# Optimization experiments

Hardware: AMD Instinct MI355X
Metric: run time of the kernel (lower is better)

Reference implementation:

```python
import jax, jax.numpy as jnp
import numpy as np

P, F_IN, HG, C, T, E, HOUT = 4096, 64, 64, 64, 32, 65536, 12
LEAKY_SLOPE = 0.2
LN_EPS = 1e-5


def setup_inputs() -> dict:
    key = jax.random.key(0)
    ks = jax.random.split(key, 14)
    g = lambda k, shape, scale: (jax.random.normal(k, shape, jnp.float32) * scale)
    return {
        "X": jax.random.normal(ks[0], (1, P, F_IN, T), jnp.float32),
        "edge_index": jax.random.randint(ks[1], (T, 2, E), 0, P, jnp.int32),
        # GATv2 params (single head)
        "Wl": g(ks[2], (F_IN, HG), 0.1),
        "Wr": g(ks[3], (F_IN, HG), 0.1),
        "att": g(ks[4], (HG,), 0.1),
        "gat_b": g(ks[5], (HG,), 0.02),
        # 1x1 time conv (HG -> C) and 1x1 residual conv (F_IN -> C)
        "W_time": g(ks[6], (C, HG), 0.1),
        "b_time": g(ks[7], (C,), 0.02),
        "W_res": g(ks[8], (C, F_IN), 0.1),
        "b_res": g(ks[9], (C,), 0.02),
        # LayerNorm over channel dim C
        "ln_g": jnp.ones((C,), jnp.float32),
        "ln_b": jnp.zeros((C,), jnp.float32),
        # final conv: Conv2d(in=T, out=HOUT, kernel=(1, C)) -> weight (HOUT, T, C)
        "W_final": g(ks[10], (HOUT, T, C), 0.05),
        "b_final": g(ks[11], (HOUT,), 0.02),
    }


def reference(X, edge_index, Wl, Wr, att, gat_b, W_time, b_time, W_res, b_res,
              ln_g, ln_b, W_final, b_final):
    Pn = X.shape[1]

    def gat_t(x, edges):
        # x: (P, F_IN), edges: (2, E) with edges[0]=src j, edges[1]=dst i
        src, dst = edges[0], edges[1]
        hl = x @ Wl                      # (P, HG) messages
        hr = x @ Wr                      # (P, HG) query side
        e = jax.nn.leaky_relu(hl[src] + hr[dst], LEAKY_SLOPE) @ att  # (E,)
        emax = jax.ops.segment_max(e, dst, num_segments=Pn)
        ex = jnp.exp(e - emax[dst])
        den = jax.ops.segment_sum(ex, dst, num_segments=Pn)
        alpha = ex / den[dst]            # softmax over in-edges of each dst
        return jax.ops.segment_sum(alpha[:, None] * hl[src], dst,
                                   num_segments=Pn) + gat_b  # (P, HG)

    xs = jnp.moveaxis(X[0], -1, 0)                     # (T, P, F_IN)
    X_hat = jax.nn.relu(jax.vmap(gat_t)(xs, edge_index))  # (T, P, HG)

    th = jnp.einsum('tph,ch->tpc', X_hat, W_time) + b_time  # time conv 1x1
    rs = jnp.einsum('tpf,cf->tpc', xs, W_res) + b_res       # residual conv 1x1
    y = jax.nn.relu(th + rs)                                 # (T, P, C)

    mu = jnp.mean(y, axis=-1, keepdims=True)
    var = jnp.var(y, axis=-1, keepdims=True)
    yn = (y - mu) * jax.lax.rsqrt(var + LN_EPS) * ln_g + ln_b  # (T, P, C)

    # final conv: in-channels = T, kernel (1, C) -> contract over t and c
    out = jnp.einsum('tpc,otc->po', yn, W_final) + b_final     # (P, HOUT)
    return out[None]                                           # (1, P, HOUT)
```

## Files before the change

### kernel.cpp

```cpp
#include <hip/hip_runtime.h>
#include <math.h>

#define NP 4096
#define F_IN 64
#define HG 64
#define NC 64
#define NT 32
#define NE 65536
#define HOUT 12
#define LEAKY 0.2f
#define LN_EPS 1e-5f
#define CAPC 32

template <int CTRL>
__device__ __forceinline__ float dppadd(float v, float x) {
    int r = __builtin_amdgcn_update_dpp(0, __builtin_bit_cast(int, x), CTRL, 0xF, 0xF, false);
    return v + __builtin_bit_cast(float, r);
}
__device__ __forceinline__ float rowsum16(float v) {
    v = dppadd<0x128>(v, v);
    v = dppadd<0x124>(v, v);
    v = dppadd<0x122>(v, v);
    v = dppadd<0x121>(v, v);
    return v;
}
__device__ __forceinline__ float laneXorSum(float v) {
    v += __shfl_xor(v, 16, 64);
    v += __shfl_xor(v, 32, 64);
    return v;
}

#define FMA4(Acomp, B, r)                                                     \
    acc[r][0] += (Acomp) * (B).x; acc[r][1] += (Acomp) * (B).y;               \
    acc[r][2] += (Acomp) * (B).z; acc[r][3] += (Acomp) * (B).w;

__global__ __launch_bounds__(256) void k_front(const float* __restrict__ X,
        const float* __restrict__ Wl, const float* __restrict__ Wr,
        const float* __restrict__ W_res, const float* __restrict__ b_res,
        const float* __restrict__ W_time,
        const int* __restrict__ EI,
        float* __restrict__ hl, float* __restrict__ hr, float* __restrict__ rs,
        float* __restrict__ wtT,
        int* __restrict__ cnt, unsigned short* __restrict__ scap) {
    __shared__ float smem[8960];
    int b = blockIdx.x;
    int tid = threadIdx.x;
    if (b < 512) {
        unsigned short (*buck)[CAPC] = (unsigned short (*)[CAPC])smem;
        int* cnts = (int*)(smem + 8192);
        int t = (b & 7) + 8 * ((b >> 3) & 3);
        int rem = b >> 5;
        int c = rem & 1, r = rem >> 1;
        cnts[tid] = 0; cnts[tid + 256] = 0;
        __syncthreads();
        const int4* srcA = (const int4*)(EI + (size_t)t * 2 * NE) + c * (NE / 8);
        const int4* dstA = (const int4*)(EI + (size_t)t * 2 * NE + NE) + c * (NE / 8);
        for (int i = tid; i < NE / 8; i += 256) {
            int4 s = srcA[i];
            int4 d = dstA[i];
            if ((d.x >> 9) == r) { int lo = d.x & 511; int sl = atomicAdd(&cnts[lo], 1); if (sl < CAPC) buck[lo][sl] = (unsigned short)s.x; }
            if ((d.y >> 9) == r) { int lo = d.y & 511; int sl = atomicAdd(&cnts[lo], 1); if (sl < CAPC) buck[lo][sl] = (unsigned short)s.y; }
            if ((d.z >> 9) == r) { int lo = d.z & 511; int sl = atomicAdd(&cnts[lo], 1); if (sl < CAPC) buck[lo][sl] = (unsigned short)s.z; }
            if ((d.w >> 9) == r) { int lo = d.w & 511; int sl = atomicAdd(&cnts[lo], 1); if (sl < CAPC) buck[lo][sl] = (unsigned short)s.w; }
        }
        __syncthreads();
        int obase = ((t * 2 + c) << 12) + (r << 9);
        cnt[obase + tid] = cnts[tid];
        cnt[obase + tid + 256] = cnts[tid + 256];
        unsigned int* dstw = (unsigned int*)(scap + (size_t)obase * CAPC);
        const unsigned int* srcw = (const unsigned int*)buck;
        for (int i = tid; i < 512 * CAPC / 2; i += 256)
            dstw[i] = srcw[i];
    } else if (b < 2560) {
        float (*xs)[F_IN][36] = (float (*)[F_IN][36])smem;
        float (*bk)[68] = (float (*)[68])(smem + 4608);
        int p0 = (b - 512) * 2;
        const float4* Xp = (const float4*)(X + (size_t)p0 * F_IN * NT);
        for (int i4 = tid; i4 < 1024; i4 += 256) {
            int pp = i4 >> 9, f = (i4 >> 3) & 63, t0 = (i4 & 7) * 4;
            *(float4*)&xs[pp][f][t0] = Xp[i4];
        }
        int ng = tid & 15, pp = (tid >> 4) & 1, tg = tid >> 5;
        int n0 = ng * 4, t0 = tg * 4;
        {
            const float4* B4 = (const float4*)Wl;
            for (int i4 = tid; i4 < 1024; i4 += 256)
                *(float4*)&bk[i4 >> 4][(i4 & 15) * 4] = B4[i4];
            __syncthreads();
            float acc[4][4];
#pragma unroll
            for (int i = 0; i < 4; ++i)
#pragma unroll
                for (int j2 = 0; j2 < 4; ++j2) acc[i][j2] = 0.f;
#pragma unroll 8
            for (int f = 0; f < F_IN; ++f) {
                float4 B = *(const float4*)&bk[f][n0];
                float4 A = *(const float4*)&xs[pp][f][t0];
                FMA4(A.x, B, 0) FMA4(A.y, B, 1) FMA4(A.z, B, 2) FMA4(A.w, B, 3)
            }
#pragma unroll
            for (int i = 0; i < 4; ++i) {
                float4 v;
                v.x = acc[i][0]; v.y = acc[i][1]; v.z = acc[i][2]; v.w = acc[i][3];
                *(float4*)&hl[((size_t)(t0 + i) * NP + p0 + pp) * HG + n0] = v;
            }
            __syncthreads();
        }
        {
            const float4* B4 = (const float4*)Wr;
            for (int i4 = tid; i4 < 1024; i4 += 256)
                *(float4*)&bk[i4 >> 4][(i4 & 15) * 4] = B4[i4];
            __syncthreads();
            float acc[4][4];
#pragma unroll
            for (int i = 0; i < 4; ++i)
#pragma unroll
                for (int j2 = 0; j2 < 4; ++j2) acc[i][j2] = 0.f;
#pragma unroll 8
            for (int f = 0; f < F_IN; ++f) {
                float4 B = *(const float4*)&bk[f][n0];
                float4 A = *(const float4*)&xs[pp][f][t0];
                FMA4(A.x, B, 0) FMA4(A.y, B, 1) FMA4(A.z, B, 2) FMA4(A.w, B, 3)
            }
#pragma unroll
            for (int i = 0; i < 4; ++i) {
                float4 v;
                v.x = acc[i][0]; v.y = acc[i][1]; v.z = acc[i][2]; v.w = acc[i][3];
                *(float4*)&hr[((size_t)(t0 + i) * NP + p0 + pp) * HG + n0] = v;
            }
            __syncthreads();
        }
        {
            for (int i = tid; i < F_IN * NC; i += 256) {
                int c = i >> 6, f = i & 63;
                bk[f][c] = W_res[i];
            }
            __syncthreads();
            float4 br4 = *(const float4*)&b_res[n0];
            float acc[4][4];
#pragma unroll
            for (int i = 0; i < 4; ++i) {
                acc[i][0] = br4.x; acc[i][1] = br4.y; acc[i][2] = br4.z; acc[i][3] = br4.w;
            }
#pragma unroll 8
            for (int f = 0; f < F_IN; ++f) {
                float4 B = *(const float4*)&bk[f][n0];
                float4 A = *(const float4*)&xs[pp][f][t0];
                FMA4(A.x, B, 0) FMA4(A.y, B, 1) FMA4(A.z, B, 2) FMA4(A.w, B, 3)
            }
#pragma unroll
            for (int i = 0; i < 4; ++i) {
                float4 v;
                v.x = acc[i][0]; v.y = acc[i][1]; v.z = acc[i][2]; v.w = acc[i][3];
                *(float4*)&rs[((size_t)(t0 + i) * NP + p0 + pp) * NC + n0] = v;
            }
        }
    } else {
        int i = (b - 2560) * 256 + tid;
        wtT[i] = W_time[(i & 63) * 64 + (i >> 6)];
    }
}

__global__ __launch_bounds__(256) void k_gat(const float* __restrict__ hl,
        const float* __restrict__ hr, const float* __restrict__ rs,
        const int* __restrict__ cnt, const unsigned short* __restrict__ scap,
        const float* __restrict__ att, const float* __restrict__ gat_b,
        const float* __restrict__ wtT, const float* __restrict__ b_time,
        const float* __restrict__ ln_g, const float* __restrict__ ln_b,
        const float* __restrict__ Wf, float* __restrict__ pout) {
    __shared__ int sidx[4][64];
    __shared__ float xbuf[4][64];
    int b = blockIdx.x;
    int t = (b & 7) + 8 * (b >> 10);
    int pc = (b >> 3) & 127;
    int ws = threadIdx.x >> 6;
    int lane = threadIdx.x & 63;
    int row = lane >> 4;
    int cg = lane & 15;
    int c0 = cg * 4;
    const float* hlt = hl + (size_t)t * NP * HG;
    float4 at4 = *(const float4*)&att[c0];
    float4 gb4 = *(const float4*)&gat_b[c0];
    float4 bt4 = *(const float4*)&b_time[c0];
    float4 lg  = *(const float4*)&ln_g[c0];
    float4 lb  = *(const float4*)&ln_b[c0];
    float4 wreg[16];
    {
        const float4* wq = (const float4*)wtT + (size_t)(row * 16) * (HG / 4) + cg;
#pragma unroll
        for (int i = 0; i < 16; ++i) wreg[i] = wq[i * (HG / 4)];
    }
    float4 wf0 = *(const float4*)&Wf[((size_t)(3 * row + 0) * NT + t) * NC + c0];
    float4 wf1 = *(const float4*)&Wf[((size_t)(3 * row + 1) * NT + t) * NC + c0];
    float4 wf2 = *(const float4*)&Wf[((size_t)(3 * row + 2) * NT + t) * NC + c0];

    for (int q = 0; q < 8; ++q) {
        int p = pc * 32 + ws * 8 + q;
        size_t nbase = ((size_t)t * NP + p) * HG;
        float4 r4 = *(const float4*)&hr[nbase + c0];
        int d0 = cnt[((t * 2 + 0) << 12) + p]; d0 = (d0 < CAPC) ? d0 : CAPC;
        int d1 = cnt[((t * 2 + 1) << 12) + p]; d1 = (d1 < CAPC) ? d1 : CAPC;
        int deg = d0 + d1;
        const unsigned short* s0 = scap + ((size_t)(((t * 2 + 0) << 12) + p)) * CAPC;
        const unsigned short* s1 = scap + ((size_t)(((t * 2 + 1) << 12) + p)) * CAPC;
        int li = (lane < deg) ? lane : 0;
        int f1 = (li >= d0);
        int idx = f1 ? (li - d0) : li;
        sidx[ws][lane] = (int)(f1 ? s1 : s0)[idx];
        float l = 0.f;
        float4 acc = {0.f, 0.f, 0.f, 0.f};
        int nfull = deg & ~7;
        int j = 0;
        for (; j < nfull; j += 8) {
            int src0 = sidx[ws][j + row];
            int src1 = sidx[ws][j + 4 + row];
            float4 h0 = *(const float4*)&hlt[((size_t)src0 << 6) + c0];
            float4 h1 = *(const float4*)&hlt[((size_t)src1 << 6) + c0];
            float4 z0, z1;
            z0.x = h0.x + r4.x; z0.y = h0.y + r4.y; z0.z = h0.z + r4.z; z0.w = h0.w + r4.w;
            z1.x = h1.x + r4.x; z1.y = h1.y + r4.y; z1.z = h1.z + r4.z; z1.w = h1.w + r4.w;
            z0.x = fmaxf(z0.x, LEAKY * z0.x); z0.y = fmaxf(z0.y, LEAKY * z0.y);
            z0.z = fmaxf(z0.z, LEAKY * z0.z); z0.w = fmaxf(z0.w, LEAKY * z0.w);
            z1.x = fmaxf(z1.x, LEAKY * z1.x); z1.y = fmaxf(z1.y, LEAKY * z1.y);
            z1.z = fmaxf(z1.z, LEAKY * z1.z); z1.w = fmaxf(z1.w, LEAKY * z1.w);
            float e0 = rowsum16(z0.x * at4.x + z0.y * at4.y + z0.z * at4.z + z0.w * at4.w);
            float e1 = rowsum16(z1.x * at4.x + z1.y * at4.y + z1.z * at4.z + z1.w * at4.w);
            float w0 = __expf(e0);
            float w1 = __expf(e1);
            l += w0 + w1;
            acc.x += w0 * h0.x + w1 * h1.x;
            acc.y += w0 * h0.y + w1 * h1.y;
            acc.z += w0 * h0.z + w1 * h1.z;
            acc.w += w0 * h0.w + w1 * h1.w;
        }
        for (; j < deg; j += 4) {
            int jj = j + row;
            int src = sidx[ws][(jj < deg) ? jj : 0];
            float4 ha = *(const float4*)&hlt[((size_t)src << 6) + c0];
            float4 za;
            za.x = ha.x + r4.x; za.y = ha.y + r4.y; za.z = ha.z + r4.z; za.w = ha.w + r4.w;
            za.x = fmaxf(za.x, LEAKY * za.x);
            za.y = fmaxf(za.y, LEAKY * za.y);
            za.z = fmaxf(za.z, LEAKY * za.z);
            za.w = fmaxf(za.w, LEAKY * za.w);
            float ep = za.x * at4.x + za.y * at4.y + za.z * at4.z + za.w * at4.w;
            float e = rowsum16(ep);
            float w = __expf(e);
            w = (jj < deg) ? w : 0.f;
            l += w;
            acc.x += w * ha.x; acc.y += w * ha.y; acc.z += w * ha.z; acc.w += w * ha.w;
        }
        float lt = laneXorSum(l);
        acc.x = laneXorSum(acc.x);
        acc.y = laneXorSum(acc.y);
        acc.z = laneXorSum(acc.z);
        acc.w = laneXorSum(acc.w);
        float inv = (deg > 0) ? (1.0f / lt) : 0.f;
        float4 xh;
        xh.x = fmaxf(acc.x * inv + gb4.x, 0.f);
        xh.y = fmaxf(acc.y * inv + gb4.y, 0.f);
        xh.z = fmaxf(acc.z * inv + gb4.z, 0.f);
        xh.w = fmaxf(acc.w * inv + gb4.w, 0.f);
        if (row == 0) *(float4*)&xbuf[ws][c0] = xh;
        float4 y4 = {0.f, 0.f, 0.f, 0.f};
#pragma unroll
        for (int i = 0; i < 16; ++i) {
            float xf = xbuf[ws][row * 16 + i];
            y4.x += xf * wreg[i].x; y4.y += xf * wreg[i].y;
            y4.z += xf * wreg[i].z; y4.w += xf * wreg[i].w;
        }
        y4.x = laneXorSum(y4.x); y4.y = laneXorSum(y4.y);
        y4.z = laneXorSum(y4.z); y4.w = laneXorSum(y4.w);
        float4 rs4 = *(const float4*)&rs[((size_t)t * NP + p) * NC + c0];
        float y0 = fmaxf(y4.x + bt4.x + rs4.x, 0.f);
        float y1 = fmaxf(y4.y + bt4.y + rs4.y, 0.f);
        float y2 = fmaxf(y4.z + bt4.z + rs4.z, 0.f);
        float y3 = fmaxf(y4.w + bt4.w + rs4.w, 0.f);
        float s  = rowsum16(y0 + y1 + y2 + y3);
        float ss = rowsum16(y0 * y0 + y1 * y1 + y2 * y2 + y3 * y3);
        float mu = s * (1.f / 64.f);
        float var = ss * (1.f / 64.f) - mu * mu;
        float rsd = rsqrtf(var + LN_EPS);
        float n0 = (y0 - mu) * rsd * lg.x + lb.x;
        float n1 = (y1 - mu) * rsd * lg.y + lb.y;
        float n2 = (y2 - mu) * rsd * lg.z + lb.z;
        float n3 = (y3 - mu) * rsd * lg.w + lb.w;
        float o0 = n0 * wf0.x + n1 * wf0.y + n2 * wf0.z + n3 * wf0.w;
        float o1 = n0 * wf1.x + n1 * wf1.y + n2 * wf1.z + n3 * wf1.w;
        float o2 = n0 * wf2.x + n1 * wf2.y + n2 * wf2.z + n3 * wf2.w;
        o0 = rowsum16(o0); o1 = rowsum16(o1); o2 = rowsum16(o2);
        if (cg == 0) {
            float* pp = pout + ((size_t)t * NP + p) * HOUT + 3 * row;
            pp[0] = o0; pp[1] = o1; pp[2] = o2;
        }
    }
}

__global__ __launch_bounds__(256) void k_out(const float* __restrict__ pout,
        const float* __restrict__ bf, float* __restrict__ out) {
    int k = blockIdx.x * 256 + threadIdx.x;
    float s = bf[k % HOUT];
#pragma unroll 8
    for (int t = 0; t < NT; ++t) s += pout[(size_t)t * (NP * HOUT) + k];
    out[k] = s;
}

extern "C" void kernel_launch(void* const* d_in, const int* in_sizes, int n_in,
                              void* d_out, int out_size, void* d_ws, size_t ws_size,
                              hipStream_t stream) {
    const float* X      = (const float*)d_in[0];
    const int*   EI     = (const int*)d_in[1];
    const float* Wl     = (const float*)d_in[2];
    const float* Wr     = (const float*)d_in[3];
    const float* att    = (const float*)d_in[4];
    const float* gat_b  = (const float*)d_in[5];
    const float* W_time = (const float*)d_in[6];
    const float* b_time = (const float*)d_in[7];
    const float* W_res  = (const float*)d_in[8];
    const float* b_res  = (const float*)d_in[9];
    const float* ln_g   = (const float*)d_in[10];
    const float* ln_b   = (const float*)d_in[11];
    const float* Wf     = (const float*)d_in[12];
    const float* bf     = (const float*)d_in[13];
    float* out = (float*)d_out;

    char* ws = (char*)d_ws;
    const size_t MB = 1024 * 1024;
    float* hl   = (float*)(ws);
    float* hr   = (float*)(ws + 32 * MB);
    float* rs   = (float*)(ws + 64 * MB);
    float* wtT  = (float*)(ws + 96 * MB);
    int*   cnt  = (int*)  (ws + 97 * MB);
    unsigned short* scap = (unsigned short*)(ws + 98 * MB);
    float* pout = (float*)(ws + 114 * MB);

    k_front<<<2576, 256, 0, stream>>>(X, Wl, Wr, W_res, b_res, W_time, EI,
                                      hl, hr, rs, wtT, cnt, scap);
    k_gat  <<<4096, 256, 0, stream>>>(hl, hr, rs, cnt, scap, att, gat_b,
                                      wtT, b_time, ln_g, ln_b, Wf, pout);
    k_out  <<<NP * HOUT / 256, 256, 0, stream>>>(pout, bf, out);
}
```

Before: 285.0 us.

## Restructure GAT kernel into phased per-warp batches with LDS weights and coalesced output

k_gat now prefetches the degrees and source indices for all 8 nodes of a wavefront into LDS up front. It then runs the attention aggregation for all 8 nodes, and afterwards does the time-conv matmul as one batched pass that reads the transposed W_time from LDS instead of holding 16 float4 registers per thread. Final per-node outputs are staged in LDS and written to pout as one contiguous store per wavefront instead of scattered 3-float writes. k_front's X tile padding changes from 36 to 40 floats. The intent is lower register pressure, better latency hiding and fewer small global stores, at the cost of more LDS use per block.

```diff
diff --git a/kernel.cpp b/kernel.cpp
--- a/kernel.cpp
+++ b/kernel.cpp
@@ -42,7 +42,7 @@
         float* __restrict__ hl, float* __restrict__ hr, float* __restrict__ rs,
         float* __restrict__ wtT,
         int* __restrict__ cnt, unsigned short* __restrict__ scap) {
-    __shared__ float smem[8960];
+    __shared__ float smem[9472];
     int b = blockIdx.x;
     int tid = threadIdx.x;
     if (b < 512) {
@@ -72,8 +72,8 @@
         for (int i = tid; i < 512 * CAPC / 2; i += 256)
             dstw[i] = srcw[i];
     } else if (b < 2560) {
-        float (*xs)[F_IN][36] = (float (*)[F_IN][36])smem;
-        float (*bk)[68] = (float (*)[68])(smem + 4608);
+        float (*xs)[F_IN][40] = (float (*)[F_IN][40])smem;
+        float (*bk)[68] = (float (*)[68])(smem + 5120);
         int p0 = (b - 512) * 2;
         const float4* Xp = (const float4*)(X + (size_t)p0 * F_IN * NT);
         for (int i4 = tid; i4 < 1024; i4 += 256) {
@@ -168,52 +168,60 @@
         const float* __restrict__ wtT, const float* __restrict__ b_time,
         const float* __restrict__ ln_g, const float* __restrict__ ln_b,
         const float* __restrict__ Wf, float* __restrict__ pout) {
-    __shared__ int sidx[4][64];
-    __shared__ float xbuf[4][64];
+    __shared__ int sidx[4][8][64];
+    __shared__ float xbuf[4][8][64];
+    __shared__ int sdeg[4][8];
+    __shared__ float wt[64][68];
     int b = blockIdx.x;
     int t = (b & 7) + 8 * (b >> 10);
     int pc = (b >> 3) & 127;
-    int ws = threadIdx.x >> 6;
-    int lane = threadIdx.x & 63;
+    int tid = threadIdx.x;
+    int ws = tid >> 6;
+    int lane = tid & 63;
     int row = lane >> 4;
     int cg = lane & 15;
     int c0 = cg * 4;
-    const float* hlt = hl + (size_t)t * NP * HG;
+    const float4* w4s = (const float4*)wtT;
+    for (int i4 = tid; i4 < 1024; i4 += 256)
+        *(float4*)&wt[i4 >> 4][(i4 & 15) * 4] = w4s[i4];
+    __syncthreads();
     float4 at4 = *(const float4*)&att[c0];
     float4 gb4 = *(const float4*)&gat_b[c0];
     float4 bt4 = *(const float4*)&b_time[c0];
     float4 lg  = *(const float4*)&ln_g[c0];
     float4 lb  = *(const float4*)&ln_b[c0];
-    float4 wreg[16];
-    {
-        const float4* wq = (const float4*)wtT + (size_t)(row * 16) * (HG / 4) + cg;
-#pragma unroll
-        for (int i = 0; i < 16; ++i) wreg[i] = wq[i * (HG / 4)];
-    }
     float4 wf0 = *(const float4*)&Wf[((size_t)(3 * row + 0) * NT + t) * NC + c0];
     float4 wf1 = *(const float4*)&Wf[((size_t)(3 * row + 1) * NT + t) * NC + c0];
     float4 wf2 = *(const float4*)&Wf[((size_t)(3 * row + 2) * NT + t) * NC + c0];
-
+    int p0 = pc * 32 + ws * 8;
+    const int* cb0 = cnt + ((t * 2 + 0) << 12) + p0;
+    const int* cb1 = cnt + ((t * 2 + 1) << 12) + p0;
+    const unsigned short* sb0 = scap + ((size_t)(((t * 2 + 0) << 12) + p0)) * CAPC;
+    const unsigned short* sb1 = scap + ((size_t)(((t * 2 + 1) << 12) + p0)) * CAPC;
+#pragma unroll
     for (int q = 0; q < 8; ++q) {
-        int p = pc * 32 + ws * 8 + q;
-        size_t nbase = ((size_t)t * NP + p) * HG;
-        float4 r4 = *(const float4*)&hr[nbase + c0];
-        int d0 = cnt[((t * 2 + 0) << 12) + p]; d0 = (d0 < CAPC) ? d0 : CAPC;
-        int d1 = cnt[((t * 2 + 1) << 12) + p]; d1 = (d1 < CAPC) ? d1 : CAPC;
+        int d0 = cb0[q]; d0 = (d0 < CAPC) ? d0 : CAPC;
+        int d1 = cb1[q]; d1 = (d1 < CAPC) ? d1 : CAPC;
         int deg = d0 + d1;
-        const unsigned short* s0 = scap + ((size_t)(((t * 2 + 0) << 12) + p)) * CAPC;
-        const unsigned short* s1 = scap + ((size_t)(((t * 2 + 1) << 12) + p)) * CAPC;
+        if (lane == 0) sdeg[ws][q] = deg;
         int li = (lane < deg) ? lane : 0;
         int f1 = (li >= d0);
         int idx = f1 ? (li - d0) : li;
-        sidx[ws][lane] = (int)(f1 ? s1 : s0)[idx];
+        const unsigned short* sp = f1 ? (sb1 + q * CAPC) : (sb0 + q * CAPC);
+        sidx[ws][q][lane] = (int)sp[idx];
+    }
+    const float* hlt = hl + (size_t)t * NP * HG;
+    for (int q = 0; q < 8; ++q) {
+        int p = p0 + q;
+        float4 r4 = *(const float4*)&hr[((size_t)t * NP + p) * HG + c0];
+        int deg = sdeg[ws][q];
         float l = 0.f;
         float4 acc = {0.f, 0.f, 0.f, 0.f};
         int nfull = deg & ~7;
         int j = 0;
         for (; j < nfull; j += 8) {
-            int src0 = sidx[ws][j + row];
-            int src1 = sidx[ws][j + 4 + row];
+            int src0 = sidx[ws][q][j + row];
+            int src1 = sidx[ws][q][j + 4 + row];
             float4 h0 = *(const float4*)&hlt[((size_t)src0 << 6) + c0];
             float4 h1 = *(const float4*)&hlt[((size_t)src1 << 6) + c0];
             float4 z0, z1;
@@ -235,7 +243,7 @@
         }
         for (; j < deg; j += 4) {
             int jj = j + row;
-            int src = sidx[ws][(jj < deg) ? jj : 0];
+            int src = sidx[ws][q][(jj < deg) ? jj : 0];
             float4 ha = *(const float4*)&hlt[((size_t)src << 6) + c0];
             float4 za;
             za.x = ha.x + r4.x; za.y = ha.y + r4.y; za.z = ha.z + r4.z; za.w = ha.w + r4.w;
@@ -261,21 +269,38 @@
         xh.y = fmaxf(acc.y * inv + gb4.y, 0.f);
         xh.z = fmaxf(acc.z * inv + gb4.z, 0.f);
         xh.w = fmaxf(acc.w * inv + gb4.w, 0.f);
-        if (row == 0) *(float4*)&xbuf[ws][c0] = xh;
-        float4 y4 = {0.f, 0.f, 0.f, 0.f};
-#pragma unroll
-        for (int i = 0; i < 16; ++i) {
-            float xf = xbuf[ws][row * 16 + i];
-            y4.x += xf * wreg[i].x; y4.y += xf * wreg[i].y;
-            y4.z += xf * wreg[i].z; y4.w += xf * wreg[i].w;
-        }
-        y4.x = laneXorSum(y4.x); y4.y = laneXorSum(y4.y);
-        y4.z = laneXorSum(y4.z); y4.w = laneXorSum(y4.w);
-        float4 rs4 = *(const float4*)&rs[((size_t)t * NP + p) * NC + c0];
-        float y0 = fmaxf(y4.x + bt4.x + rs4.x, 0.f);
-        float y1 = fmaxf(y4.y + bt4.y + rs4.y, 0.f);
-        float y2 = fmaxf(y4.z + bt4.z + rs4.z, 0.f);
-        float y3 = fmaxf(y4.w + bt4.w + rs4.w, 0.f);
+        if (row == 0) *(float4*)&xbuf[ws][q][c0] = xh;
+    }
+    float4 y[8];
+#pragma unroll
+    for (int q = 0; q < 8; ++q) { y[q].x = 0.f; y[q].y = 0.f; y[q].z = 0.f; y[q].w = 0.f; }
+#pragma unroll
+    for (int i4 = 0; i4 < 4; ++i4) {
+        int h0 = row * 16 + i4 * 4;
+        float4 w0 = *(const float4*)&wt[h0 + 0][c0];
+        float4 w1 = *(const float4*)&wt[h0 + 1][c0];
+        float4 w2 = *(const float4*)&wt[h0 + 2][c0];
+        float4 w3 = *(const float4*)&wt[h0 + 3][c0];
+#pragma unroll
+        for (int q = 0; q < 8; ++q) {
+            float4 xf = *(const float4*)&xbuf[ws][q][h0];
+            y[q].x += xf.x * w0.x + xf.y * w1.x + xf.z * w2.x + xf.w * w3.x;
+            y[q].y += xf.x * w0.y + xf.y * w1.y + xf.z * w2.y + xf.w * w3.y;
+            y[q].z += xf.x * w0.z + xf.y * w1.z + xf.z * w2.z + xf.w * w3.z;
+            y[q].w += xf.x * w0.w + xf.y * w1.w + xf.z * w2.w + xf.w * w3.w;
+        }
+    }
+#pragma unroll
+    for (int q = 0; q < 8; ++q) {
+        float ya = laneXorSum(y[q].x);
+        float yb = laneXorSum(y[q].y);
+        float yc = laneXorSum(y[q].z);
+        float yd = laneXorSum(y[q].w);
+        float4 rs4 = *(const float4*)&rs[((size_t)t * NP + p0 + q) * NC + c0];
+        float y0 = fmaxf(ya + bt4.x + rs4.x, 0.f);
+        float y1 = fmaxf(yb + bt4.y + rs4.y, 0.f);
+        float y2 = fmaxf(yc + bt4.z + rs4.z, 0.f);
+        float y3 = fmaxf(yd + bt4.w + rs4.w, 0.f);
         float s  = rowsum16(y0 + y1 + y2 + y3);
         float ss = rowsum16(y0 * y0 + y1 * y1 + y2 * y2 + y3 * y3);
         float mu = s * (1.f / 64.f);
@@ -290,10 +315,14 @@
         float o2 = n0 * wf2.x + n1 * wf2.y + n2 * wf2.z + n3 * wf2.w;
         o0 = rowsum16(o0); o1 = rowsum16(o1); o2 = rowsum16(o2);
         if (cg == 0) {
-            float* pp = pout + ((size_t)t * NP + p) * HOUT + 3 * row;
-            pp[0] = o0; pp[1] = o1; pp[2] = o2;
-        }
-    }
+            xbuf[ws][q][3 * row + 0] = o0;
+            xbuf[ws][q][3 * row + 1] = o1;
+            xbuf[ws][q][3 * row + 2] = o2;
+        }
+    }
+    float* pb = pout + ((size_t)t * NP + p0) * HOUT;
+    for (int k = lane; k < 96; k += 64)
+        pb[k] = xbuf[ws][k / 12][k % 12];
 }
 
 __global__ __launch_bounds__(256) void k_out(const float* __restrict__ pout,
```

Result: slower. 323.5 us (+13.5%).
